# Kernel tuning notes

Hardware: AMD Instinct MI355X
Metric: run time of the kernel (lower is better)

Reference implementation:

```python
import jax, jax.numpy as jnp
import numpy as np

SCALE = 16.0
TEMP = 0.07
EPS = 1e-8


def setup_inputs() -> dict:
    key = jax.random.key(0)
    k0, k1, k2, k3, k4 = jax.random.split(key, 5)
    B, D, h, w = 16, 128, 48, 48
    feats_a = jax.random.normal(k0, (B, D, h, w), jnp.float32)
    feats_b = jax.random.normal(k1, (B, D, h, w), jnp.float32)
    eye = jnp.eye(3, dtype=jnp.float32)
    # near-identity homographies (must be invertible)
    Hs_a = eye[None] + 0.02 * jax.random.normal(k2, (B, 3, 3), jnp.float32)
    Hs_b = eye[None] + 0.02 * jax.random.normal(k3, (B, 3, 3), jnp.float32)
    # near-identity affine with a small translation (in large-image pixels)
    M_a_b = jnp.array([[1.0, 0.0, 24.0], [0.0, 1.0, -16.0]], jnp.float32) \
        + 0.01 * jax.random.normal(k4, (2, 3), jnp.float32)
    return {"feats_a": feats_a, "feats_b": feats_b, "Hs_a": Hs_a, "Hs_b": Hs_b, "M_a_b": M_a_b}


def _transform_matrix(Hs_a, Hs_b, M_a_b):
    # Feat_A -> Img_A -> Large_A -> Large_B -> Img_B -> Feat_B
    B = Hs_a.shape[0]
    dt = Hs_a.dtype
    M3 = jnp.concatenate([M_a_b, jnp.array([[0.0, 0.0, 1.0]], dt)], axis=0)  # (3,3)
    S = jnp.diag(jnp.array([SCALE, SCALE, 1.0], dt))
    S_inv = jnp.diag(jnp.array([1.0 / SCALE, 1.0 / SCALE, 1.0], dt))
    Ha_inv = jnp.linalg.inv(Hs_a)  # (B,3,3)
    T = S_inv[None] @ Hs_b @ M3[None] @ Ha_inv @ S[None]
    return T


def _bilinear_sample(feats, grid):
    # feats (B,D,H,W); grid (B,h,w,2) normalized to [-1,1], align_corners=True,
    # zero padding for out-of-range samples (matches F.grid_sample).
    B, D, H, W = feats.shape
    h, w = grid.shape[1], grid.shape[2]
    ix = (grid[..., 0] + 1.0) * 0.5 * (W - 1)  # (B,h,w)
    iy = (grid[..., 1] + 1.0) * 0.5 * (H - 1)
    x0 = jnp.floor(ix); y0 = jnp.floor(iy)
    wx1 = ix - x0; wx0 = 1.0 - wx1
    wy1 = iy - y0; wy0 = 1.0 - wy1
    feats_flat = feats.reshape(B, D, H * W)

    def gather(xi, yi):
        valid = (xi >= 0) & (xi <= W - 1) & (yi >= 0) & (yi <= H - 1)
        xc = jnp.clip(xi, 0, W - 1).astype(jnp.int32)
        yc = jnp.clip(yi, 0, H - 1).astype(jnp.int32)
        idx = (yc * W + xc).reshape(B, -1)  # (B, h*w)
        v = jnp.take_along_axis(feats_flat, idx[:, None, :], axis=2)  # (B,D,h*w)
        return v * valid.reshape(B, 1, -1).astype(feats.dtype)

    out = (gather(x0, y0) * (wx0 * wy0).reshape(B, 1, -1)
           + gather(x0 + 1, y0) * (wx1 * wy0).reshape(B, 1, -1)
           + gather(x0, y0 + 1) * (wx0 * wy1).reshape(B, 1, -1)
           + gather(x0 + 1, y0 + 1) * (wx1 * wy1).reshape(B, 1, -1))
    return out.reshape(B, D, h, w)


def reference(feats_a, feats_b, Hs_a, Hs_b, M_a_b):
    B, D, h, w = feats_a.shape
    N = h * w
    H_b, W_b = feats_b.shape[2], feats_b.shape[3]
    T = _transform_matrix(Hs_a, Hs_b, M_a_b)  # (B,3,3)

    # homogeneous pixel grid of feats_a: (3, N)
    gy, gx = jnp.meshgrid(jnp.arange(h, dtype=jnp.float32), jnp.arange(w, dtype=jnp.float32), indexing='ij')
    coords = jnp.stack([gx.ravel(), gy.ravel(), jnp.ones(N, jnp.float32)], axis=0)  # (3,N)
    new = jnp.einsum('bij,jn->bin', T, coords)  # (B,3,N)
    z = new[:, 2, :] + EPS
    x_norm = 2.0 * (new[:, 0, :] / z) / (W_b - 1) - 1.0  # (B,N)
    y_norm = 2.0 * (new[:, 1, :] / z) / (H_b - 1) - 1.0
    grid = jnp.stack([x_norm, y_norm], axis=-1).reshape(B, h, w, 2)
    valid_mask = ((grid[..., 0] >= -1) & (grid[..., 0] <= 1)
                  & (grid[..., 1] >= -1) & (grid[..., 1] <= 1)).astype(jnp.float32)  # (B,h,w)

    warped_b = _bilinear_sample(feats_b, grid)  # (B,D,h,w)

    fa = feats_a.reshape(B, D, N).transpose(0, 2, 1)   # (B,N,D)
    wb = warped_b.reshape(B, D, N).transpose(0, 2, 1)  # (B,N,D)
    # F.normalize: x / max(||x||, eps) with eps=1e-12
    fa = fa / jnp.maximum(jnp.linalg.norm(fa, axis=2, keepdims=True), 1e-12)
    wb = wb / jnp.maximum(jnp.linalg.norm(wb, axis=2, keepdims=True), 1e-12)

    logits = jnp.einsum('bnd,bmd->bnm', fa, wb) / TEMP  # (B,N,N)
    # cross-entropy with labels = diagonal
    lse = jax.nn.logsumexp(logits, axis=-1)  # (B,N)
    diag = jnp.einsum('bnn->bn', logits)     # (B,N)
    loss_per = lse - diag                    # (B,N)

    mask = valid_mask.reshape(B, N)
    num_valid = mask.sum()
    total = (loss_per * mask).sum()
    return jnp.where(num_valid > 0, total / jnp.maximum(num_valid, 1.0), 0.0)
```

## Files before the change

kernel.cpp:

```cpp
#include <hip/hip_runtime.h>
#include <math.h>

#define B_ 16
#define D_ 128
#define HH 48
#define WW 48
#define N_ 2304
#define SCALE_ 16.0f
#define INV_TEMP 14.285714285714286f
#define L2E_TEMP 20.60992915555662f
#define EPS_ 1e-8f
#define KP 136
#define SPLIT 4
#define JT_PER 9

typedef __attribute__((ext_vector_type(8))) short bf16x8;
typedef __attribute__((ext_vector_type(16))) float f32x16;

__device__ __forceinline__ short f2bf(float f) {
    union { float f; unsigned u; } v; v.f = f;
    unsigned r = v.u + 0x7FFFu + ((v.u >> 16) & 1u);
    return (short)(r >> 16);
}
__device__ __forceinline__ float bf2f(short s) {
    union { unsigned u; float f; } v;
    v.u = ((unsigned)(unsigned short)s) << 16;
    return v.f;
}

__global__ __launch_bounds__(512) void k_prep(const float* __restrict__ fa,
                                              const float* __restrict__ fb,
                                              const float* __restrict__ Ha,
                                              const float* __restrict__ Hb,
                                              const float* __restrict__ Mab,
                                              float* __restrict__ maskA,
                                              short* __restrict__ faN,
                                              short* __restrict__ wbN) {
    __shared__ short sbA[D_][65];
    __shared__ short sbW[D_][65];
    __shared__ float part[8][2][64];
    __shared__ float rn[2][64];
    const int b = blockIdx.y;
    const int n0 = blockIdx.x * 64;
    const int tid = threadIdx.x;
    const int nl = tid & 63, dg = tid >> 6;
    const int n = n0 + nl;

    float T[9];
    {
        const float* A = Ha + b * 9;
        const float* Bm = Hb + b * 9;
        float c00 = A[4] * A[8] - A[5] * A[7];
        float c01 = A[5] * A[6] - A[3] * A[8];
        float c02 = A[3] * A[7] - A[4] * A[6];
        float id = 1.f / (A[0] * c00 + A[1] * c01 + A[2] * c02);
        float inv[9] = { c00 * id, (A[2] * A[7] - A[1] * A[8]) * id, (A[1] * A[5] - A[2] * A[4]) * id,
                         c01 * id, (A[0] * A[8] - A[2] * A[6]) * id, (A[2] * A[3] - A[0] * A[5]) * id,
                         c02 * id, (A[1] * A[6] - A[0] * A[7]) * id, (A[0] * A[4] - A[1] * A[3]) * id };
        float M3[9] = {Mab[0], Mab[1], Mab[2], Mab[3], Mab[4], Mab[5], 0.f, 0.f, 1.f};
        float P1[9], P2[9];
        for (int i = 0; i < 3; ++i)
            for (int j = 0; j < 3; ++j) {
                float s = 0.f;
                for (int k = 0; k < 3; ++k) s += Bm[i * 3 + k] * M3[k * 3 + j];
                P1[i * 3 + j] = s;
            }
        for (int i = 0; i < 3; ++i)
            for (int j = 0; j < 3; ++j) {
                float s = 0.f;
                for (int k = 0; k < 3; ++k) s += P1[i * 3 + k] * inv[k * 3 + j];
                P2[i * 3 + j] = s;
            }
        const float sc[3] = {SCALE_, SCALE_, 1.f};
        for (int i = 0; i < 3; ++i)
            for (int j = 0; j < 3; ++j) T[i * 3 + j] = P2[i * 3 + j] * sc[j] / sc[i];
    }

    const float gx = (float)(n % WW), gy = (float)(n / WW);
    const float X = T[0] * gx + T[1] * gy + T[2];
    const float Y = T[3] * gx + T[4] * gy + T[5];
    const float z = T[6] * gx + T[7] * gy + T[8] + EPS_;
    const float xn = 2.f * (X / z) / (float)(WW - 1) - 1.f;
    const float yn = 2.f * (Y / z) / (float)(HH - 1) - 1.f;
    const float msk = (xn >= -1.f && xn <= 1.f && yn >= -1.f && yn <= 1.f) ? 1.f : 0.f;
    const float ix = (xn + 1.f) * 0.5f * (float)(WW - 1);
    const float iy = (yn + 1.f) * 0.5f * (float)(HH - 1);
    const float x0f = floorf(ix), y0f = floorf(iy);
    const float wx1 = ix - x0f, wx0 = 1.f - wx1;
    const float wy1 = iy - y0f, wy0 = 1.f - wy1;
    const bool vx0 = (x0f >= 0.f) && (x0f <= 47.f);
    const bool vx1 = (x0f + 1.f >= 0.f) && (x0f + 1.f <= 47.f);
    const bool vy0 = (y0f >= 0.f) && (y0f <= 47.f);
    const bool vy1 = (y0f + 1.f >= 0.f) && (y0f + 1.f <= 47.f);
    const float w00 = (vx0 && vy0) ? wx0 * wy0 : 0.f;
    const float w01 = (vx1 && vy0) ? wx1 * wy0 : 0.f;
    const float w10 = (vx0 && vy1) ? wx0 * wy1 : 0.f;
    const float w11 = (vx1 && vy1) ? wx1 * wy1 : 0.f;
    const int x0c = (int)fminf(fmaxf(x0f, 0.f), 47.f);
    const int x1c = (int)fminf(fmaxf(x0f + 1.f, 0.f), 47.f);
    const int y0c = (int)fminf(fmaxf(y0f, 0.f), 47.f);
    const int y1c = (int)fminf(fmaxf(y0f + 1.f, 0.f), 47.f);
    const int o00 = y0c * WW + x0c, o01 = y0c * WW + x1c;
    const int o10 = y1c * WW + x0c, o11 = y1c * WW + x1c;

    const float* fab = fa + (size_t)b * D_ * N_;
    const float* fbb = fb + (size_t)b * D_ * N_;
    float sA = 0.f, sW = 0.f;
    for (int dd = 0; dd < 16; ++dd) {
        int d = dg * 16 + dd;
        const float* p = fbb + (size_t)d * N_;
        float w = w00 * p[o00] + w01 * p[o01] + w10 * p[o10] + w11 * p[o11];
        float a = fab[(size_t)d * N_ + n];
        sbA[d][nl] = f2bf(a);
        sbW[d][nl] = f2bf(w);
        sA += a * a;
        sW += w * w;
    }
    part[dg][0][nl] = sA;
    part[dg][1][nl] = sW;
    __syncthreads();
    if (tid < 64) {
        float ta = 0.f, tw = 0.f;
        for (int g = 0; g < 8; ++g) { ta += part[g][0][tid]; tw += part[g][1][tid]; }
        rn[0][tid] = 1.f / fmaxf(sqrtf(ta), 1e-12f);
        rn[1][tid] = 1.f / fmaxf(sqrtf(tw), 1e-12f);
        maskA[b * N_ + n0 + tid] = msk;
    }
    __syncthreads();
    const int c = tid & 15, rr = tid >> 4;
    for (int p2 = 0; p2 < 2; ++p2) {
        int r = rr + p2 * 32;
        float sa = rn[0][r], sw = rn[1][r];
        bf16x8 oa, ow;
        for (int j = 0; j < 8; ++j) {
            oa[j] = f2bf(bf2f(sbA[c * 8 + j][r]) * sa);
            ow[j] = f2bf(bf2f(sbW[c * 8 + j][r]) * sw);
        }
        *(bf16x8*)(faN + (size_t)(b * N_ + n0 + r) * D_ + c * 8) = oa;
        *(bf16x8*)(wbN + (size_t)(b * N_ + n0 + r) * D_ + c * 8) = ow;
    }
}

__global__ __launch_bounds__(256) void k_loss(const short* __restrict__ faN,
                                              const short* __restrict__ wbN,
                                              float* __restrict__ Zbuf,
                                              float* __restrict__ dgbuf) {
    __shared__ short a_t[64 * KP];
    __shared__ short b_t[64 * KP];
    __shared__ float s_Z[64];
    __shared__ float s_dg[64];
    const int bx = blockIdx.x, cs = blockIdx.y, b = blockIdx.z;
    const int tid = threadIdx.x;
    const int n0 = bx * 64;
    const int c = tid & 15, r0 = tid >> 4;

    for (int p = 0; p < 4; ++p) {
        int r = p * 16 + r0;
        *(bf16x8*)(a_t + r * KP + c * 8) =
            *(const bf16x8*)(faN + (size_t)(b * N_ + n0 + r) * D_ + c * 8);
    }
    if (tid < 64) { s_Z[tid] = 0.f; s_dg[tid] = 0.f; }
    __syncthreads();

    const int lane = tid & 63, wv = tid >> 6;
    const int rq = wv >> 1, cq = wv & 1;
    const int l31 = lane & 31, h = lane >> 5;

    bf16x8 afr[8];
    {
        const short* ap = a_t + (rq * 32 + l31) * KP + h * 8;
        for (int ks = 0; ks < 8; ++ks) afr[ks] = *(const bf16x8*)(ap + ks * 16);
    }
    float Z[16];
    for (int i = 0; i < 16; ++i) Z[i] = 0.f;
    const bool hasDiag = (bx / JT_PER == cs);

    for (int q = 0; q < JT_PER; ++q) {
        const int jt = cs * JT_PER + q;
        __syncthreads();
        for (int p = 0; p < 4; ++p) {
            int r = p * 16 + r0;
            *(bf16x8*)(b_t + r * KP + c * 8) =
                *(const bf16x8*)(wbN + (size_t)(b * N_ + jt * 64 + r) * D_ + c * 8);
        }
        __syncthreads();

        const short* bp = b_t + (cq * 32 + l31) * KP + h * 8;
        f32x16 C;
        for (int i = 0; i < 16; ++i) C[i] = 0.f;
        for (int ks = 0; ks < 8; ++ks) {
            bf16x8 bfr = *(const bf16x8*)(bp + ks * 16);
            C = __builtin_amdgcn_mfma_f32_32x32x16_bf16(afr[ks], bfr, C, 0, 0, 0);
        }
        for (int i = 0; i < 16; ++i)
            Z[i] += exp2f(fmaf(C[i], L2E_TEMP, -L2E_TEMP));

        if (jt == bx) {
            int gcol_l = cq * 32 + l31;
            for (int i = 0; i < 16; ++i) {
                int rl = rq * 32 + (i & 3) + 8 * (i >> 2) + 4 * h;
                if (gcol_l == rl) s_dg[rl] = INV_TEMP * C[i];
            }
        }
    }
    for (int i = 0; i < 16; ++i) {
        float zz = Z[i];
        zz += __shfl_xor(zz, 1);
        zz += __shfl_xor(zz, 2);
        zz += __shfl_xor(zz, 4);
        zz += __shfl_xor(zz, 8);
        zz += __shfl_xor(zz, 16);
        Z[i] = zz;
    }
    if (l31 == 0) {
        for (int i = 0; i < 16; ++i) {
            int rl = rq * 32 + (i & 3) + 8 * (i >> 2) + 4 * h;
            atomicAdd(&s_Z[rl], Z[i]);
        }
    }
    __syncthreads();
    if (tid < 64) {
        atomicAdd(&Zbuf[b * N_ + n0 + tid], s_Z[tid]);
        if (hasDiag) dgbuf[b * N_ + n0 + tid] = s_dg[tid];
    }
}

__global__ __launch_bounds__(256) void k_pass2(const float* __restrict__ maskA,
                                               const float* __restrict__ Zbuf,
                                               const float* __restrict__ dgbuf,
                                               float* __restrict__ acc) {
    const int idx = blockIdx.x * 256 + threadIdx.x;
    const float m = maskA[idx];
    float lossv = (logf(Zbuf[idx]) + INV_TEMP - dgbuf[idx]) * m;
    float cm = m;
    for (int off = 1; off < 64; off <<= 1) {
        lossv += __shfl_xor(lossv, off);
        cm += __shfl_xor(cm, off);
    }
    __shared__ float s[8];
    const int wv = threadIdx.x >> 6;
    if ((threadIdx.x & 63) == 0) { s[wv * 2] = lossv; s[wv * 2 + 1] = cm; }
    __syncthreads();
    if (threadIdx.x == 0) {
        atomicAdd(&acc[0], s[0] + s[2] + s[4] + s[6]);
        atomicAdd(&acc[1], s[1] + s[3] + s[5] + s[7]);
    }
}

__global__ void k_final(const float* __restrict__ acc, float* __restrict__ out) {
    float t = acc[0], c = acc[1];
    out[0] = (c > 0.f) ? t / fmaxf(c, 1.f) : 0.f;
}

extern "C" void kernel_launch(void* const* d_in, const int* in_sizes, int n_in,
                              void* d_out, int out_size, void* d_ws, size_t ws_size,
                              hipStream_t stream) {
    const float* fa = (const float*)d_in[0];
    const float* fb = (const float*)d_in[1];
    const float* Ha = (const float*)d_in[2];
    const float* Hb = (const float*)d_in[3];
    const float* M = (const float*)d_in[4];
    float* out = (float*)d_out;

    float* wsf = (float*)d_ws;
    float* accp = wsf;
    float* Zbuf = wsf + 2;
    float* dgbuf = Zbuf + B_ * N_;
    float* maskA = dgbuf + B_ * N_;
    short* faN = (short*)(maskA + B_ * N_);
    short* wbN = faN + (size_t)B_ * N_ * D_;

    hipMemsetAsync(wsf, 0, (2 + B_ * N_) * sizeof(float), stream);
    hipLaunchKernelGGL(k_prep, dim3(N_ / 64, B_), dim3(512), 0, stream,
                       fa, fb, Ha, Hb, M, maskA, faN, wbN);
    hipLaunchKernelGGL(k_loss, dim3(N_ / 64, SPLIT, B_), dim3(256), 0, stream,
                       faN, wbN, Zbuf, dgbuf);
    hipLaunchKernelGGL(k_pass2, dim3(B_ * N_ / 256), dim3(256), 0, stream,
                       maskA, Zbuf, dgbuf, accp);
    hipLaunchKernelGGL(k_final, dim3(1), dim3(1), 0, stream, accp, out);
}
```

Measured before the change: 159.5 us.

## Pre-swizzle bf16 operands into MFMA fragment layout and drop LDS staging

The prep kernel now writes normalized features directly in the per-lane MFMA fragment order, so the loss kernel loads A and B fragments straight from global memory without LDS tiles or barriers. Each wave computes two 32-row blocks that share one B fragment, and the column split doubles to 8 slices. Per-row partial sums go to separate slices that pass2 adds up, replacing the memset and global atomics. The cost is B fragments being read from global/L2 with no LDS reuse across waves, plus more partial-sum traffic.

```diff
diff --git a/kernel.cpp b/kernel.cpp
--- a/kernel.cpp
+++ b/kernel.cpp
@@ -6,13 +6,13 @@
 #define HH 48
 #define WW 48
 #define N_ 2304
+#define NC 72
 #define SCALE_ 16.0f
 #define INV_TEMP 14.285714285714286f
 #define L2E_TEMP 20.60992915555662f
 #define EPS_ 1e-8f
-#define KP 136
-#define SPLIT 4
-#define JT_PER 9
+#define SPLIT 8
+#define JC_PER 9
 
 typedef __attribute__((ext_vector_type(8))) short bf16x8;
 typedef __attribute__((ext_vector_type(16))) float f32x16;
@@ -22,28 +22,28 @@
     unsigned r = v.u + 0x7FFFu + ((v.u >> 16) & 1u);
     return (short)(r >> 16);
 }
-__device__ __forceinline__ float bf2f(short s) {
-    union { unsigned u; float f; } v;
-    v.u = ((unsigned)(unsigned short)s) << 16;
-    return v.f;
-}
-
-__global__ __launch_bounds__(512) void k_prep(const float* __restrict__ fa,
+
+__device__ __forceinline__ size_t frag_off(int b, int c, int ks, int lane) {
+    return ((((size_t)b * NC + c) * 8 + ks) << 9) + (size_t)lane * 8;
+}
+
+__global__ __launch_bounds__(256) void k_prep(const float* __restrict__ fa,
                                               const float* __restrict__ fb,
                                               const float* __restrict__ Ha,
                                               const float* __restrict__ Hb,
                                               const float* __restrict__ Mab,
                                               float* __restrict__ maskA,
-                                              short* __restrict__ faN,
-                                              short* __restrict__ wbN) {
-    __shared__ short sbA[D_][65];
-    __shared__ short sbW[D_][65];
-    __shared__ float part[8][2][64];
-    __shared__ float rn[2][64];
+                                              short* __restrict__ faF,
+                                              short* __restrict__ wbF) {
+    __shared__ float sbA[D_][33];
+    __shared__ float sbW[D_][33];
+    __shared__ float part[8][2][32];
+    __shared__ float rn[2][32];
     const int b = blockIdx.y;
-    const int n0 = blockIdx.x * 64;
+    const int rb = blockIdx.x;
+    const int n0 = rb * 32;
     const int tid = threadIdx.x;
-    const int nl = tid & 63, dg = tid >> 6;
+    const int nl = tid & 31, dg = tid >> 5;
     const int n = n0 + nl;
 
     float T[9];
@@ -111,15 +111,15 @@
         const float* p = fbb + (size_t)d * N_;
         float w = w00 * p[o00] + w01 * p[o01] + w10 * p[o10] + w11 * p[o11];
         float a = fab[(size_t)d * N_ + n];
-        sbA[d][nl] = f2bf(a);
-        sbW[d][nl] = f2bf(w);
+        sbA[d][nl] = a;
+        sbW[d][nl] = w;
         sA += a * a;
         sW += w * w;
     }
     part[dg][0][nl] = sA;
     part[dg][1][nl] = sW;
     __syncthreads();
-    if (tid < 64) {
+    if (tid < 32) {
         float ta = 0.f, tw = 0.f;
         for (int g = 0; g < 8; ++g) { ta += part[g][0][tid]; tw += part[g][1][tid]; }
         rn[0][tid] = 1.f / fmaxf(sqrtf(ta), 1e-12f);
@@ -127,111 +127,109 @@
         maskA[b * N_ + n0 + tid] = msk;
     }
     __syncthreads();
-    const int c = tid & 15, rr = tid >> 4;
-    for (int p2 = 0; p2 < 2; ++p2) {
-        int r = rr + p2 * 32;
-        float sa = rn[0][r], sw = rn[1][r];
+    const int lane = tid & 63, wv = tid >> 6;
+    const int r = lane & 31, h = lane >> 5;
+    const float sa = rn[0][r], sw = rn[1][r];
+    for (int t = 0; t < 2; ++t) {
+        const int ks = wv + t * 4;
         bf16x8 oa, ow;
         for (int j = 0; j < 8; ++j) {
-            oa[j] = f2bf(bf2f(sbA[c * 8 + j][r]) * sa);
-            ow[j] = f2bf(bf2f(sbW[c * 8 + j][r]) * sw);
-        }
-        *(bf16x8*)(faN + (size_t)(b * N_ + n0 + r) * D_ + c * 8) = oa;
-        *(bf16x8*)(wbN + (size_t)(b * N_ + n0 + r) * D_ + c * 8) = ow;
-    }
-}
-
-__global__ __launch_bounds__(256) void k_loss(const short* __restrict__ faN,
-                                              const short* __restrict__ wbN,
-                                              float* __restrict__ Zbuf,
-                                              float* __restrict__ dgbuf) {
-    __shared__ short a_t[64 * KP];
-    __shared__ short b_t[64 * KP];
-    __shared__ float s_Z[64];
-    __shared__ float s_dg[64];
-    const int bx = blockIdx.x, cs = blockIdx.y, b = blockIdx.z;
+            int d = ks * 16 + h * 8 + j;
+            oa[j] = f2bf(sbA[d][r] * sa);
+            ow[j] = f2bf(sbW[d][r] * sw);
+        }
+        size_t off = frag_off(b, rb, ks, lane);
+        *(bf16x8*)(faF + off) = oa;
+        *(bf16x8*)(wbF + off) = ow;
+    }
+}
+
+__global__ __launch_bounds__(256, 2) void k_loss(const short* __restrict__ faF,
+                                                 const short* __restrict__ wbF,
+                                                 float* __restrict__ Zpart,
+                                                 float* __restrict__ dgbuf) {
+    __shared__ float s_Z[256];
+    const int bx = blockIdx.x;
+    const int cs = blockIdx.y;
+    const int b = blockIdx.z;
     const int tid = threadIdx.x;
-    const int n0 = bx * 64;
-    const int c = tid & 15, r0 = tid >> 4;
-
-    for (int p = 0; p < 4; ++p) {
-        int r = p * 16 + r0;
-        *(bf16x8*)(a_t + r * KP + c * 8) =
-            *(const bf16x8*)(faN + (size_t)(b * N_ + n0 + r) * D_ + c * 8);
-    }
-    if (tid < 64) { s_Z[tid] = 0.f; s_dg[tid] = 0.f; }
-    __syncthreads();
-
     const int lane = tid & 63, wv = tid >> 6;
-    const int rq = wv >> 1, cq = wv & 1;
     const int l31 = lane & 31, h = lane >> 5;
-
-    bf16x8 afr[8];
-    {
-        const short* ap = a_t + (rq * 32 + l31) * KP + h * 8;
-        for (int ks = 0; ks < 8; ++ks) afr[ks] = *(const bf16x8*)(ap + ks * 16);
-    }
-    float Z[16];
-    for (int i = 0; i < 16; ++i) Z[i] = 0.f;
-    const bool hasDiag = (bx / JT_PER == cs);
-
-    for (int q = 0; q < JT_PER; ++q) {
-        const int jt = cs * JT_PER + q;
-        __syncthreads();
-        for (int p = 0; p < 4; ++p) {
-            int r = p * 16 + r0;
-            *(bf16x8*)(b_t + r * KP + c * 8) =
-                *(const bf16x8*)(wbN + (size_t)(b * N_ + jt * 64 + r) * D_ + c * 8);
-        }
-        __syncthreads();
-
-        const short* bp = b_t + (cq * 32 + l31) * KP + h * 8;
-        f32x16 C;
-        for (int i = 0; i < 16; ++i) C[i] = 0.f;
+    const int rc0 = bx * 8 + wv * 2, rc1 = rc0 + 1;
+
+    bf16x8 a0[8], a1[8];
+    #pragma unroll
+    for (int ks = 0; ks < 8; ++ks) {
+        a0[ks] = *(const bf16x8*)(faF + frag_off(b, rc0, ks, lane));
+        a1[ks] = *(const bf16x8*)(faF + frag_off(b, rc1, ks, lane));
+    }
+    float Z0[16], Z1[16];
+    #pragma unroll
+    for (int i = 0; i < 16; ++i) { Z0[i] = 0.f; Z1[i] = 0.f; }
+
+    for (int q = 0; q < JC_PER; ++q) {
+        const int jc = cs * JC_PER + q;
+        const short* bbase = wbF + frag_off(b, jc, 0, lane);
+        f32x16 C0, C1;
+        #pragma unroll
+        for (int i = 0; i < 16; ++i) { C0[i] = 0.f; C1[i] = 0.f; }
+        #pragma unroll
         for (int ks = 0; ks < 8; ++ks) {
-            bf16x8 bfr = *(const bf16x8*)(bp + ks * 16);
-            C = __builtin_amdgcn_mfma_f32_32x32x16_bf16(afr[ks], bfr, C, 0, 0, 0);
-        }
-        for (int i = 0; i < 16; ++i)
-            Z[i] += exp2f(fmaf(C[i], L2E_TEMP, -L2E_TEMP));
-
-        if (jt == bx) {
-            int gcol_l = cq * 32 + l31;
+            bf16x8 bf = *(const bf16x8*)(bbase + ks * 512);
+            C0 = __builtin_amdgcn_mfma_f32_32x32x16_bf16(a0[ks], bf, C0, 0, 0, 0);
+            C1 = __builtin_amdgcn_mfma_f32_32x32x16_bf16(a1[ks], bf, C1, 0, 0, 0);
+        }
+        #pragma unroll
+        for (int i = 0; i < 16; ++i) {
+            Z0[i] += exp2f(fmaf(C0[i], L2E_TEMP, -L2E_TEMP));
+            Z1[i] += exp2f(fmaf(C1[i], L2E_TEMP, -L2E_TEMP));
+        }
+        if (jc == rc0) {
+            #pragma unroll
             for (int i = 0; i < 16; ++i) {
-                int rl = rq * 32 + (i & 3) + 8 * (i >> 2) + 4 * h;
-                if (gcol_l == rl) s_dg[rl] = INV_TEMP * C[i];
-            }
-        }
-    }
+                int rl = (i & 3) + 8 * (i >> 2) + 4 * h;
+                if (l31 == rl) dgbuf[b * N_ + rc0 * 32 + rl] = INV_TEMP * C0[i];
+            }
+        }
+        if (jc == rc1) {
+            #pragma unroll
+            for (int i = 0; i < 16; ++i) {
+                int rl = (i & 3) + 8 * (i >> 2) + 4 * h;
+                if (l31 == rl) dgbuf[b * N_ + rc1 * 32 + rl] = INV_TEMP * C1[i];
+            }
+        }
+    }
+    #pragma unroll
     for (int i = 0; i < 16; ++i) {
-        float zz = Z[i];
-        zz += __shfl_xor(zz, 1);
-        zz += __shfl_xor(zz, 2);
-        zz += __shfl_xor(zz, 4);
-        zz += __shfl_xor(zz, 8);
-        zz += __shfl_xor(zz, 16);
-        Z[i] = zz;
+        float z0 = Z0[i], z1 = Z1[i];
+        z0 += __shfl_xor(z0, 1);  z1 += __shfl_xor(z1, 1);
+        z0 += __shfl_xor(z0, 2);  z1 += __shfl_xor(z1, 2);
+        z0 += __shfl_xor(z0, 4);  z1 += __shfl_xor(z1, 4);
+        z0 += __shfl_xor(z0, 8);  z1 += __shfl_xor(z1, 8);
+        z0 += __shfl_xor(z0, 16); z1 += __shfl_xor(z1, 16);
+        Z0[i] = z0; Z1[i] = z1;
     }
     if (l31 == 0) {
+        #pragma unroll
         for (int i = 0; i < 16; ++i) {
-            int rl = rq * 32 + (i & 3) + 8 * (i >> 2) + 4 * h;
-            atomicAdd(&s_Z[rl], Z[i]);
-        }
-    }
-    __syncthreads();
-    if (tid < 64) {
-        atomicAdd(&Zbuf[b * N_ + n0 + tid], s_Z[tid]);
-        if (hasDiag) dgbuf[b * N_ + n0 + tid] = s_dg[tid];
-    }
+            int rl = (i & 3) + 8 * (i >> 2) + 4 * h;
+            s_Z[wv * 64 + rl] = Z0[i];
+            s_Z[wv * 64 + 32 + rl] = Z1[i];
+        }
+    }
+    __syncthreads();
+    Zpart[((size_t)cs * B_ + b) * N_ + bx * 256 + tid] = s_Z[tid];
 }
 
 __global__ __launch_bounds__(256) void k_pass2(const float* __restrict__ maskA,
-                                               const float* __restrict__ Zbuf,
+                                               const float* __restrict__ Zpart,
                                                const float* __restrict__ dgbuf,
                                                float* __restrict__ acc) {
     const int idx = blockIdx.x * 256 + threadIdx.x;
+    float Zs = 0.f;
+    for (int s = 0; s < SPLIT; ++s) Zs += Zpart[(size_t)s * B_ * N_ + idx];
     const float m = maskA[idx];
-    float lossv = (logf(Zbuf[idx]) + INV_TEMP - dgbuf[idx]) * m;
+    float lossv = (logf(Zs) + INV_TEMP - dgbuf[idx]) * m;
     float cm = m;
     for (int off = 1; off < 64; off <<= 1) {
         lossv += __shfl_xor(lossv, off);
@@ -264,18 +262,18 @@
 
     float* wsf = (float*)d_ws;
     float* accp = wsf;
-    float* Zbuf = wsf + 2;
-    float* dgbuf = Zbuf + B_ * N_;
-    float* maskA = dgbuf + B_ * N_;
-    short* faN = (short*)(maskA + B_ * N_);
-    short* wbN = faN + (size_t)B_ * N_ * D_;
-
-    hipMemsetAsync(wsf, 0, (2 + B_ * N_) * sizeof(float), stream);
-    hipLaunchKernelGGL(k_prep, dim3(N_ / 64, B_), dim3(512), 0, stream,
-                       fa, fb, Ha, Hb, M, maskA, faN, wbN);
-    hipLaunchKernelGGL(k_loss, dim3(N_ / 64, SPLIT, B_), dim3(256), 0, stream,
-                       faN, wbN, Zbuf, dgbuf);
+    float* maskA = wsf + 2;
+    float* dgbuf = maskA + B_ * N_;
+    float* Zpart = dgbuf + B_ * N_;
+    short* faF = (short*)(Zpart + (size_t)SPLIT * B_ * N_);
+    short* wbF = faF + (size_t)B_ * NC * 8 * 512;
+
+    hipMemsetAsync(accp, 0, 2 * sizeof(float), stream);
+    hipLaunchKernelGGL(k_prep, dim3(NC, B_), dim3(256), 0, stream,
+                       fa, fb, Ha, Hb, M, maskA, faF, wbF);
+    hipLaunchKernelGGL(k_loss, dim3(9, SPLIT, B_), dim3(256), 0, stream,
+                       faF, wbF, Zpart, dgbuf);
     hipLaunchKernelGGL(k_pass2, dim3(B_ * N_ / 256), dim3(256), 0, stream,
-                       maskA, Zbuf, dgbuf, accp);
+                       maskA, Zpart, dgbuf, accp);
     hipLaunchKernelGGL(k_final, dim3(1), dim3(1), 0, stream, accp, out);
 }
```

After: 167.0 us. 1.05x slower.
